# Kernel tuning notes

Measured on AMD Instinct MI355X. Metric: run time of the kernel, lower is better.

Reference implementation:

```python
import math
import jax, jax.numpy as jnp
import numpy as np

IN_CH = 64
NUM_ANCHOR = 4
MAP_H, MAP_W = 96, 96
BATCH = 8
BN_EPS = 1e-5


def _conv2d(x, w, b, padding, dilation):
    # x: [B,C,H,W], w: [O,I,kh,kw] (OIHW)
    y = jax.lax.conv_general_dilated(
        x, w, window_strides=(1, 1),
        padding=((padding, padding), (padding, padding)),
        rhs_dilation=(dilation, dilation),
        dimension_numbers=('NCHW', 'OIHW', 'NCHW'))
    return y + b[None, :, None, None]


def _bn(x, gamma, beta, mean, var):
    scale = gamma / jnp.sqrt(var + BN_EPS)
    return x * scale[None, :, None, None] + (beta - mean * scale)[None, :, None, None]


def setup_inputs() -> dict:
    key = jax.random.key(0)
    ks = jax.random.split(key, 12)
    # cyclic channel-shift permutation matrices, one per anchor pass
    eye = np.eye(IN_CH, dtype=np.float32)
    shift = IN_CH // (2 * NUM_ANCHOR)
    perms = np.stack([eye[np.roll(np.arange(IN_CH), i * shift)] for i in range(2 * NUM_ANCHOR)])
    w_std = 1.0 / math.sqrt(IN_CH * 9)
    return {
        'x': jax.random.normal(ks[0], (BATCH, IN_CH, MAP_H, MAP_W), dtype=jnp.float32),
        'perms': jnp.asarray(perms),
        'dcn_w': jax.random.normal(ks[1], (IN_CH, IN_CH, 3, 3), dtype=jnp.float32) * w_std,
        'dcn_b': jax.random.normal(ks[2], (IN_CH,), dtype=jnp.float32) * 0.01,
        'conv2_w': jax.random.normal(ks[3], (IN_CH, IN_CH, 3, 3), dtype=jnp.float32) * w_std,
        'conv2_b': jax.random.normal(ks[4], (IN_CH,), dtype=jnp.float32) * 0.01,
        'conv3_w': jax.random.normal(ks[5], (IN_CH, IN_CH, 3, 3), dtype=jnp.float32) * w_std,
        'conv3_b': jax.random.normal(ks[6], (IN_CH,), dtype=jnp.float32) * 0.01,
        'bn_gamma': jax.random.uniform(ks[7], (3, IN_CH), dtype=jnp.float32, minval=0.5, maxval=1.5),
        'bn_beta': jax.random.normal(ks[8], (3, IN_CH), dtype=jnp.float32) * 0.1,
        'bn_mean': jax.random.normal(ks[9], (3, IN_CH), dtype=jnp.float32) * 0.1,
        'bn_var': jax.random.uniform(ks[10], (3, IN_CH), dtype=jnp.float32, minval=0.5, maxval=1.5),
    }


def reference(x, perms, dcn_w, dcn_b, conv2_w, conv2_b, conv3_w, conv3_b,
              bn_gamma, bn_beta, bn_mean, bn_var):
    h = x.shape[2]
    pad = math.ceil(h / (2 ** 1.5 + 2))  # 20 for h=96

    def conv_stack(o):
        # DCN at init (zero offsets) == plain 3x3 conv, pad=1
        o = jax.nn.relu(_bn(_conv2d(o, dcn_w, dcn_b, 1, 1), bn_gamma[0], bn_beta[0], bn_mean[0], bn_var[0]))
        o = jax.nn.relu(_bn(_conv2d(o, conv2_w, conv2_b, 2, 2), bn_gamma[1], bn_beta[1], bn_mean[1], bn_var[1]))
        o = jax.nn.relu(_bn(_conv2d(o, conv3_w, conv3_b, 2, 2), bn_gamma[2], bn_beta[2], bn_mean[2], bn_var[2]))
        return o

    outs = []
    for i in range(2 * NUM_ANCHOR):  # fixed small structural loop
        o = jnp.einsum('mn,bnhw->bmhw', perms[i], x)  # channel permutation
        if i % 2 != 0:
            o = jnp.pad(o, ((0, 0), (0, 0), (pad, pad), (pad, pad)))
        o = jnp.rot90(o, k=i % 4, axes=(-2, -1))   # ccw rotate
        o = conv_stack(o)
        o = jnp.rot90(o, k=(-i) % 4, axes=(-2, -1))  # cw rotate back
        if i % 2 != 0:
            H, W = o.shape[-2], o.shape[-1]
            sh, sw = (H - MAP_H) // 2, (W - MAP_W) // 2
            o = o[..., sh:sh + MAP_H, sw:sw + MAP_W]  # center crop
        outs.append(o)
    out_tensor = jnp.concatenate(outs, axis=1)  # [B, 8*C, H, W]
    out = jnp.max(out_tensor, axis=1, keepdims=True)
    # branch_name == 'midpoint', orientational_anchor=False -> clamped sigmoid
    return jnp.clip(jax.nn.sigmoid(out), 1e-4, 1.0 - 1e-4)
```

## Files before the change

### kernel.cpp

```cpp
#include <hip/hip_runtime.h>
#include <math.h>

#define B 8
#define C 64
#define HW 96
#define NWV 36864

typedef __attribute__((ext_vector_type(8)))  short short8;
typedef __attribute__((ext_vector_type(16))) float floatx16;

__device__ __forceinline__ unsigned short f2bf(float f) {
    unsigned int u = __float_as_uint(f);
    unsigned int r = (u + 0x7fffu + ((u >> 16) & 1u)) >> 16;
    return (unsigned short)r;
}

__device__ __forceinline__ void rotmap(int k, int ta, int tb, int& sa, int& sb) {
    switch (k) {
        case 0: sa = ta;     sb = tb;     break;
        case 1: sa = 2 - tb; sb = ta;     break;
        case 2: sa = 2 - ta; sb = 2 - tb; break;
        default: sa = tb;    sb = 2 - ta; break;
    }
}

__global__ void prep_w(const float* __restrict__ dcn_w, const float* __restrict__ c2w,
                       const float* __restrict__ c3w,
                       const float* __restrict__ gamma, const float* __restrict__ var_,
                       unsigned short* __restrict__ Wall) {
    int idx = blockIdx.x * 256 + threadIdx.x;
    if (idx >= 16 * NWV) return;
    int v = idx / NWV, rem = idx % NWV;
    int tap  = rem >> 12;
    int w12  = rem & 4095;
    int ks   = w12 >> 10;
    int cf   = (w12 >> 9) & 1;
    int lane = (w12 >> 3) & 63;
    int j    = w12 & 7;
    int co = cf * 32 + (lane & 31);
    int ci = ks * 16 + (lane >> 5) * 8 + j;
    int ta = tap / 3, tb = tap % 3;
    const float* src; int k, srcci, l;
    if (v < 8)       { k = v & 3;  srcci = (ci + 8 * v) & 63; src = dcn_w; l = 0; }
    else if (v < 12) { k = v - 8;  srcci = ci; src = c2w; l = 1; }
    else             { k = v - 12; srcci = ci; src = c3w; l = 2; }
    int sa, sb; rotmap(k, ta, tb, sa, sb);
    float s = gamma[l * 64 + co] * rsqrtf(var_[l * 64 + co] + 1e-5f);
    Wall[idx] = f2bf(src[((co * 64 + srcci) * 3 + sa) * 3 + sb] * s);
}

__global__ void prep_bias(const float* __restrict__ dcn_b, const float* __restrict__ c2b,
                          const float* __restrict__ c3b,
                          const float* __restrict__ gamma, const float* __restrict__ beta,
                          const float* __restrict__ mean, const float* __restrict__ var_,
                          float* __restrict__ biasg) {
    int t = threadIdx.x;
    if (t < 192) {
        int l = t >> 6, c = t & 63;
        const float* cb = (l == 0) ? dcn_b : ((l == 1) ? c2b : c3b);
        float s = gamma[l * 64 + c] * rsqrtf(var_[l * 64 + c] + 1e-5f);
        biasg[t] = cb[c] * s + beta[l * 64 + c] - mean[l * 64 + c] * s;
    }
}

__global__ __launch_bounds__(256) void prep_x(const float* __restrict__ in,
                                              unsigned short* __restrict__ out) {
    __shared__ float row[64 * 97];
    int by = blockIdx.x;
    int b = by / 96, y = by % 96;
    int t = threadIdx.x;
    for (int e = t; e < 6144; e += 256) {
        int c = e / 96, x = e - c * 96;
        row[c * 97 + x] = in[(((size_t)(b * 64 + c) * 96 + y) * 96) + x];
    }
    __syncthreads();
    for (int e = t; e < 6144; e += 256) {
        int x = e >> 6, c = e & 63;
        out[(((size_t)(b * 96 + y) * 96 + x) << 6) + c] = f2bf(row[c * 97 + x]);
    }
}

__global__ __launch_bounds__(256) void border_clear(unsigned short* __restrict__ buf1) {
    int idx = blockIdx.y;
    int br = (idx >> 3) * 2, b = idx & 7;
    int z = br * 8 + b;
    int i = blockIdx.x * 32 + (threadIdx.x >> 3);
    int g = threadIdx.x & 7;
    int r, c;
    if (i < 416)      { r = i / 104;              c = i % 104; }
    else if (i < 832) { int j = i - 416; r = 100 + j / 104; c = j % 104; }
    else              { int j = i - 832; r = 4 + (j >> 3); int c8 = j & 7;
                        c = (c8 < 4) ? c8 : 92 + c8; }
    uint4 zero = make_uint4(0u, 0u, 0u, 0u);
    *(uint4*)(buf1 + (size_t)z * (104 * 104 * 64) + ((size_t)(r * 104 + c) << 6) + (g << 3)) = zero;
}

__global__ __launch_bounds__(256, 2) void conv1_k(
    const unsigned short* __restrict__ xhwc, unsigned short* __restrict__ buf1,
    const unsigned short* __restrict__ Wall, const float* __restrict__ biasg) {

    __shared__ __align__(16) unsigned short xt[10 * 34 * 64];
    __shared__ __align__(16) unsigned short xpose[256 * 64];

    int zb = blockIdx.z;
    int bq = zb >> 3, b = zb & 7;
    int fy0 = blockIdx.y * 8, fx0 = blockIdx.x * 32;
    int t = threadIdx.x, lane = t & 63, wv = t >> 6;
    int n = lane & 31, kq = lane >> 5;

    const unsigned short* xb = xhwc + ((size_t)b * 96 * 96 << 6);

    for (int e = t; e < 2720; e += 256) {
        int p = e >> 3, g = e & 7;
        int yy = p / 34, xx = p - yy * 34;
        int gy = fy0 - 5 + yy, gx = fx0 - 5 + xx;
        uint4 v = make_uint4(0u, 0u, 0u, 0u);
        if ((unsigned)gy < 96u && (unsigned)gx < 96u)
            v = *(const uint4*)(xb + ((size_t)(gy * 96 + gx) << 6) + (g << 3));
        *(uint4*)(xt + (p << 6) + ((g ^ (xx & 7)) << 3)) = v;
    }

    float4 bv[2][4];
#pragma unroll
    for (int cf = 0; cf < 2; cf++)
#pragma unroll
        for (int rb = 0; rb < 4; rb++)
            bv[cf][rb] = *(const float4*)(biasg + 32 * cf + 8 * rb + 4 * kq);

    __syncthreads();

    for (int j = 0; j < 4; ++j) {
        int br = bq * 4 + j, odd = br & 1;
        int z = br * 8 + b;
        const short8* Ag = (const short8*)(Wall + (size_t)br * NWV);

        floatx16 acc[2][2];
#pragma unroll
        for (int cf = 0; cf < 2; cf++)
#pragma unroll
            for (int pf = 0; pf < 2; pf++)
#pragma unroll
                for (int i = 0; i < 16; i++) acc[cf][pf][i] = 0.f;

#pragma unroll
        for (int ks = 0; ks < 4; ks++) {
#pragma unroll
            for (int tb = 0; tb < 3; tb++) {
                short8 a[3][2];
#pragma unroll
                for (int ta = 0; ta < 3; ta++)
#pragma unroll
                    for (int cf = 0; cf < 2; cf++)
                        a[ta][cf] = Ag[(((ta * 3 + tb) * 4 + ks) * 2 + cf) * 64 + lane];
                int xx = n + tb;
                int g = ((ks * 2 + kq) ^ (xx & 7)) << 3;
                short8 bf[4];
#pragma unroll
                for (int rr = 0; rr < 4; rr++) {
                    int p = (2 * wv + rr) * 34 + xx;
                    bf[rr] = *(const short8*)(xt + (p << 6) + g);
                }
#pragma unroll
                for (int ta = 0; ta < 3; ta++)
#pragma unroll
                    for (int pf = 0; pf < 2; pf++) {
                        int rr = pf + ta;
                        acc[0][pf] = __builtin_amdgcn_mfma_f32_32x32x16_bf16(a[ta][0], bf[rr], acc[0][pf], 0, 0, 0);
                        acc[1][pf] = __builtin_amdgcn_mfma_f32_32x32x16_bf16(a[ta][1], bf[rr], acc[1][pf], 0, 0, 0);
                    }
            }
        }

        __syncthreads();
#pragma unroll
        for (int pf = 0; pf < 2; pf++) {
            int pq = (2 * wv + pf) * 32 + n;
            int key = (pq & 7) << 1;
#pragma unroll
            for (int cf = 0; cf < 2; cf++)
#pragma unroll
                for (int rb = 0; rb < 4; rb++) {
                    int u = kq + 2 * rb + 8 * cf;
                    float v0 = fmaxf(acc[cf][pf][rb * 4 + 0] + bv[cf][rb].x, 0.f);
                    float v1 = fmaxf(acc[cf][pf][rb * 4 + 1] + bv[cf][rb].y, 0.f);
                    float v2 = fmaxf(acc[cf][pf][rb * 4 + 2] + bv[cf][rb].z, 0.f);
                    float v3 = fmaxf(acc[cf][pf][rb * 4 + 3] + bv[cf][rb].w, 0.f);
                    uint2 pk = make_uint2((unsigned)f2bf(v0) | ((unsigned)f2bf(v1) << 16),
                                          (unsigned)f2bf(v2) | ((unsigned)f2bf(v3) << 16));
                    *(uint2*)((char*)xpose + pq * 128 + ((u ^ key) << 3)) = pk;
                }
        }
        __syncthreads();

        unsigned short* fb = buf1 + (size_t)z * (104 * 104 * 64);
        int lo = odd ? 0 : 4, hi = odd ? 104 : 100;
        for (int e = t; e < 2048; e += 256) {
            int px = e >> 3, g = e & 7;
            int key = (px & 7) << 1;
            uint4 v = *(const uint4*)((const char*)xpose + px * 128 + (((2 * g) ^ key) << 3));
            int lr = px >> 5, nn = px & 31;
            int f = fy0 + lr, fc = fx0 + nn;
            if (f >= lo && f < hi && fc >= lo && fc < hi)
                *(uint4*)(fb + ((size_t)(f * 104 + fc) << 6) + (g << 3)) = v;
        }
    }
}

__global__ __launch_bounds__(1024, 4) void conv23_k(
    const unsigned short* __restrict__ buf1, float* __restrict__ maxb,
    const unsigned short* __restrict__ Wall, const float* __restrict__ biasg) {

    __shared__ __align__(16) unsigned short c2out[768 * 64];
    __shared__ __align__(16) unsigned short xs[960 * 32];

    int z = blockIdx.z, br = z >> 3, odd = br & 1;
    int oy0 = blockIdx.y * 16, ox0 = blockIdx.x * 32;
    int t = threadIdx.x, lane = t & 63, wv = t >> 6;
    int n = lane & 31, kq = lane >> 5;

    const unsigned short* fb = buf1 + (size_t)z * (104 * 104 * 64);
    const short8* A2 = (const short8*)(Wall + (size_t)(8  + (br & 3)) * NWV);
    const short8* A3 = (const short8*)(Wall + (size_t)(12 + (br & 3)) * NWV);

    for (int e = t; e < 3840; e += 1024) {
        int p = e >> 2, g = e & 3;
        int yy = p / 40, xx = p - yy * 40;
        uint4 v = *(const uint4*)(fb + ((size_t)((oy0 + yy) * 104 + ox0 + xx) << 6) + (g << 3));
        *(uint4*)(xs + (p << 5) + ((g ^ (xx & 3)) << 3)) = v;
    }
    __syncthreads();

    uint4 pfv[4];
#pragma unroll
    for (int k = 0; k < 4; k++) {
        int e = t + k * 1024;
        if (e < 3840) {
            int p = e >> 2, g = e & 3;
            int yy = p / 40, xx = p - yy * 40;
            pfv[k] = *(const uint4*)(fb + ((size_t)((oy0 + yy) * 104 + ox0 + xx) << 6) + 32 + (g << 3));
        }
    }

    int ch_[2], q_[2], row2_[2], col2_[2];
#pragma unroll
    for (int jj = 0; jj < 2; jj++) {
        int ch = 2 * wv + jj;
        ch_[jj] = ch;
        int q = ch * 32 + n;
        q_[jj] = q;
        int qc = (q < 720) ? q : 719;
        int r2 = qc / 36;
        row2_[jj] = r2;
        col2_[jj] = qc - 36 * r2;
    }

    floatx16 acc2[2][2];
#pragma unroll
    for (int jj = 0; jj < 2; jj++)
#pragma unroll
        for (int cf = 0; cf < 2; cf++)
#pragma unroll
            for (int i = 0; i < 16; i++) acc2[jj][cf][i] = 0.f;

#pragma unroll
    for (int s = 0; s < 2; s++) {
        if (s == 1) {
            __syncthreads();
#pragma unroll
            for (int k = 0; k < 4; k++) {
                int e = t + k * 1024;
                if (e < 3840) {
                    int p = e >> 2, g = e & 3;
                    int xx2 = p - (p / 40) * 40;
                    *(uint4*)(xs + (p << 5) + ((g ^ (xx2 & 3)) << 3)) = pfv[k];
                }
            }
            __syncthreads();
        }
        if (ch_[0] < 23) {
#pragma unroll
            for (int kl = 0; kl < 2; kl++) {
                int ks = s * 2 + kl;
#pragma unroll
                for (int tb = 0; tb < 3; tb++) {
                    short8 a[3][2];
#pragma unroll
                    for (int ta = 0; ta < 3; ta++)
#pragma unroll
                        for (int cf = 0; cf < 2; cf++)
                            a[ta][cf] = A2[(((ta * 3 + tb) * 4 + ks) * 2 + cf) * 64 + lane];
#pragma unroll
                    for (int jj = 0; jj < 2; jj++) {
                        if (ch_[jj] < 23) {
                            int colx = col2_[jj] + 2 * tb;
                            int gsw = ((kl * 2 + kq) ^ (colx & 3)) << 3;
#pragma unroll
                            for (int ta = 0; ta < 3; ta++) {
                                int p = (row2_[jj] + 2 * ta) * 40 + colx;
                                short8 bfr = *(const short8*)(xs + (p << 5) + gsw);
                                acc2[jj][0] = __builtin_amdgcn_mfma_f32_32x32x16_bf16(a[ta][0], bfr, acc2[jj][0], 0, 0, 0);
                                acc2[jj][1] = __builtin_amdgcn_mfma_f32_32x32x16_bf16(a[ta][1], bfr, acc2[jj][1], 0, 0, 0);
                            }
                        }
                    }
                }
            }
        }
    }

    int rlo2 = (!odd && oy0 == 0)  ? 2  : 0;
    int rhi2 = (!odd && oy0 == 80) ? 18 : 20;
    int clo2 = (!odd && ox0 == 0)  ? 2  : 0;
    int chi2 = (!odd && ox0 == 64) ? 34 : 36;
    float4 bv2[2][4];
#pragma unroll
    for (int cf = 0; cf < 2; cf++)
#pragma unroll
        for (int rb = 0; rb < 4; rb++)
            bv2[cf][rb] = *(const float4*)(biasg + 64 + 32 * cf + 8 * rb + 4 * kq);

#pragma unroll
    for (int jj = 0; jj < 2; jj++) {
        if (ch_[jj] < 23 && q_[jj] < 720) {
            bool valid = (row2_[jj] >= rlo2) && (row2_[jj] < rhi2) &&
                         (col2_[jj] >= clo2) && (col2_[jj] < chi2);
            int key = col2_[jj] & 14;
#pragma unroll
            for (int cf = 0; cf < 2; cf++)
#pragma unroll
                for (int rb = 0; rb < 4; rb++) {
                    int u = kq + 2 * rb + 8 * cf;
                    float v0 = 0.f, v1 = 0.f, v2 = 0.f, v3 = 0.f;
                    if (valid) {
                        v0 = fmaxf(acc2[jj][cf][rb * 4 + 0] + bv2[cf][rb].x, 0.f);
                        v1 = fmaxf(acc2[jj][cf][rb * 4 + 1] + bv2[cf][rb].y, 0.f);
                        v2 = fmaxf(acc2[jj][cf][rb * 4 + 2] + bv2[cf][rb].z, 0.f);
                        v3 = fmaxf(acc2[jj][cf][rb * 4 + 3] + bv2[cf][rb].w, 0.f);
                    }
                    uint2 pk = make_uint2((unsigned)f2bf(v0) | ((unsigned)f2bf(v1) << 16),
                                          (unsigned)f2bf(v2) | ((unsigned)f2bf(v3) << 16));
                    *(uint2*)((char*)c2out + q_[jj] * 128 + ((u ^ key) << 3)) = pk;
                }
        }
    }
    __syncthreads();

    int r0 = wv;
    floatx16 acc3[2];
#pragma unroll
    for (int cf = 0; cf < 2; cf++)
#pragma unroll
        for (int i = 0; i < 16; i++) acc3[cf][i] = 0.f;

#pragma unroll
    for (int ks = 0; ks < 4; ks++) {
#pragma unroll
        for (int tb = 0; tb < 3; tb++) {
            short8 a[3][2];
#pragma unroll
            for (int ta = 0; ta < 3; ta++)
#pragma unroll
                for (int cf = 0; cf < 2; cf++)
                    a[ta][cf] = A3[(((ta * 3 + tb) * 4 + ks) * 2 + cf) * 64 + lane];
            int col = n + 2 * tb;
            int key = col & 14;
            int ublk = 2 * (ks * 2 + kq);
            short8 bf[3];
#pragma unroll
            for (int ta = 0; ta < 3; ta++) {
                int q = (r0 + 2 * ta) * 36 + col;
                bf[ta] = *(const short8*)((const char*)c2out + q * 128 + ((ublk ^ key) << 3));
            }
#pragma unroll
            for (int ta = 0; ta < 3; ta++) {
                acc3[0] = __builtin_amdgcn_mfma_f32_32x32x16_bf16(a[ta][0], bf[ta], acc3[0], 0, 0, 0);
                acc3[1] = __builtin_amdgcn_mfma_f32_32x32x16_bf16(a[ta][1], bf[ta], acc3[1], 0, 0, 0);
            }
        }
    }

    float4 bv3[2][4];
#pragma unroll
    for (int cf = 0; cf < 2; cf++)
#pragma unroll
        for (int rb = 0; rb < 4; rb++)
            bv3[cf][rb] = *(const float4*)(biasg + 128 + 32 * cf + 8 * rb + 4 * kq);

    float m = 0.f;
#pragma unroll
    for (int cf = 0; cf < 2; cf++)
#pragma unroll
        for (int rb = 0; rb < 4; rb++) {
            m = fmaxf(m, acc3[cf][rb * 4 + 0] + bv3[cf][rb].x);
            m = fmaxf(m, acc3[cf][rb * 4 + 1] + bv3[cf][rb].y);
            m = fmaxf(m, acc3[cf][rb * 4 + 2] + bv3[cf][rb].z);
            m = fmaxf(m, acc3[cf][rb * 4 + 3] + bv3[cf][rb].w);
        }
    m = fmaxf(m, 0.f);
    m = fmaxf(m, __shfl_xor(m, 32, 64));
    if (lane < 32)
        maxb[((size_t)z * 96 + oy0 + r0) * 96 + ox0 + n] = m;
}

__global__ void final_k(const float* __restrict__ maxb, float* __restrict__ out) {
    int i = blockIdx.x * 256 + threadIdx.x;
    if (i < B * HW * HW) {
        int b = i / 9216, yx = i - b * 9216;
        float m = 0.f;
#pragma unroll
        for (int br = 0; br < 8; br++)
            m = fmaxf(m, maxb[((size_t)(br * 8 + b)) * 9216 + yx]);
        float v = 1.f / (1.f + expf(-m));
        out[i] = fminf(fmaxf(v, 1e-4f), 1.f - 1e-4f);
    }
}


extern "C" void kernel_launch(void* const* d_in, const int* in_sizes, int n_in,
                              void* d_out, int out_size, void* d_ws, size_t ws_size,
                              hipStream_t stream) {
    const float* x     = (const float*)d_in[0];
    const float* dcn_w = (const float*)d_in[2];
    const float* dcn_b = (const float*)d_in[3];
    const float* c2w   = (const float*)d_in[4];
    const float* c2b   = (const float*)d_in[5];
    const float* c3w   = (const float*)d_in[6];
    const float* c3b   = (const float*)d_in[7];
    const float* gamma = (const float*)d_in[8];
    const float* beta  = (const float*)d_in[9];
    const float* mean  = (const float*)d_in[10];
    const float* var_  = (const float*)d_in[11];

    char* ws = (char*)d_ws;
    unsigned short* Wall = (unsigned short*)ws;
    size_t off = (size_t)16 * NWV * 2;
    float* biasg = (float*)(ws + off);            off += 1024;
    float* maxb  = (float*)(ws + off);            off += (size_t)64 * 9216 * 4;
    unsigned short* xhwc = (unsigned short*)(ws + off); off += (size_t)B * 9216 * 64 * 2;
    unsigned short* buf1 = (unsigned short*)(ws + off);

    prep_w<<<(16 * NWV + 255) / 256, 256, 0, stream>>>(dcn_w, c2w, c3w, gamma, var_, Wall);
    prep_bias<<<1, 256, 0, stream>>>(dcn_b, c2b, c3b, gamma, beta, mean, var_, biasg);
    prep_x<<<B * 96, 256, 0, stream>>>(x, xhwc);
    border_clear<<<dim3(50, 32), 256, 0, stream>>>(buf1);

    dim3 g1(4, 13, 16);
    conv1_k<<<g1, 256, 0, stream>>>(xhwc, buf1, Wall, biasg);

    dim3 g23(3, 6, 64);
    conv23_k<<<g23, 1024, 0, stream>>>(buf1, maxb, Wall, biasg);

    final_k<<<(B * HW * HW + 255) / 256, 256, 0, stream>>>(maxb, (float*)d_out);
}
```

Measured before the change: 333.2 us.

## Split conv1 per branch and halve conv23 tile height with shared LDS buffer

conv1 now launches one block per branch instead of looping over four branches per block, and reuses the input tile's LDS for the transpose staging. conv23 drops to 8 output rows per block with 512 threads and aliases the input and conv2-output LDS regions, assigning the extra conv2 row chunks to spare waves. This shrinks per-block LDS to raise occupancy and adds blocks for better CU fill, at the cost of reloading input halos more often and doing relatively more halo conv2 work per output.

```diff
diff --git a/kernel.cpp b/kernel.cpp
--- a/kernel.cpp
+++ b/kernel.cpp
@@ -100,15 +100,14 @@
     const unsigned short* __restrict__ Wall, const float* __restrict__ biasg) {
 
     __shared__ __align__(16) unsigned short xt[10 * 34 * 64];
-    __shared__ __align__(16) unsigned short xpose[256 * 64];
-
-    int zb = blockIdx.z;
-    int bq = zb >> 3, b = zb & 7;
+
+    int z = blockIdx.z, br = z >> 3, b = z & 7, odd = br & 1;
     int fy0 = blockIdx.y * 8, fx0 = blockIdx.x * 32;
     int t = threadIdx.x, lane = t & 63, wv = t >> 6;
     int n = lane & 31, kq = lane >> 5;
 
     const unsigned short* xb = xhwc + ((size_t)b * 96 * 96 << 6);
+    const short8* Ag = (const short8*)(Wall + (size_t)br * NWV);
 
     for (int e = t; e < 2720; e += 256) {
         int p = e >> 3, g = e & 7;
@@ -119,6 +118,44 @@
             v = *(const uint4*)(xb + ((size_t)(gy * 96 + gx) << 6) + (g << 3));
         *(uint4*)(xt + (p << 6) + ((g ^ (xx & 7)) << 3)) = v;
     }
+    __syncthreads();
+
+    floatx16 acc[2][2];
+#pragma unroll
+    for (int cf = 0; cf < 2; cf++)
+#pragma unroll
+        for (int pf = 0; pf < 2; pf++)
+#pragma unroll
+            for (int i = 0; i < 16; i++) acc[cf][pf][i] = 0.f;
+
+#pragma unroll
+    for (int ks = 0; ks < 4; ks++) {
+#pragma unroll
+        for (int tb = 0; tb < 3; tb++) {
+            short8 a[3][2];
+#pragma unroll
+            for (int ta = 0; ta < 3; ta++)
+#pragma unroll
+                for (int cf = 0; cf < 2; cf++)
+                    a[ta][cf] = Ag[(((ta * 3 + tb) * 4 + ks) * 2 + cf) * 64 + lane];
+            int xx = n + tb;
+            int g = ((ks * 2 + kq) ^ (xx & 7)) << 3;
+            short8 bf[4];
+#pragma unroll
+            for (int rr = 0; rr < 4; rr++) {
+                int p = (2 * wv + rr) * 34 + xx;
+                bf[rr] = *(const short8*)(xt + (p << 6) + g);
+            }
+#pragma unroll
+            for (int ta = 0; ta < 3; ta++)
+#pragma unroll
+                for (int pf = 0; pf < 2; pf++) {
+                    int rr = pf + ta;
+                    acc[0][pf] = __builtin_amdgcn_mfma_f32_32x32x16_bf16(a[ta][0], bf[rr], acc[0][pf], 0, 0, 0);
+                    acc[1][pf] = __builtin_amdgcn_mfma_f32_32x32x16_bf16(a[ta][1], bf[rr], acc[1][pf], 0, 0, 0);
+                }
+        }
+    }
 
     float4 bv[2][4];
 #pragma unroll
@@ -128,93 +165,49 @@
             bv[cf][rb] = *(const float4*)(biasg + 32 * cf + 8 * rb + 4 * kq);
 
     __syncthreads();
-
-    for (int j = 0; j < 4; ++j) {
-        int br = bq * 4 + j, odd = br & 1;
-        int z = br * 8 + b;
-        const short8* Ag = (const short8*)(Wall + (size_t)br * NWV);
-
-        floatx16 acc[2][2];
+#pragma unroll
+    for (int pf = 0; pf < 2; pf++) {
+        int pq = (2 * wv + pf) * 32 + n;
+        int key = (pq & 7) << 1;
 #pragma unroll
         for (int cf = 0; cf < 2; cf++)
 #pragma unroll
-            for (int pf = 0; pf < 2; pf++)
-#pragma unroll
-                for (int i = 0; i < 16; i++) acc[cf][pf][i] = 0.f;
-
-#pragma unroll
-        for (int ks = 0; ks < 4; ks++) {
-#pragma unroll
-            for (int tb = 0; tb < 3; tb++) {
-                short8 a[3][2];
-#pragma unroll
-                for (int ta = 0; ta < 3; ta++)
-#pragma unroll
-                    for (int cf = 0; cf < 2; cf++)
-                        a[ta][cf] = Ag[(((ta * 3 + tb) * 4 + ks) * 2 + cf) * 64 + lane];
-                int xx = n + tb;
-                int g = ((ks * 2 + kq) ^ (xx & 7)) << 3;
-                short8 bf[4];
-#pragma unroll
-                for (int rr = 0; rr < 4; rr++) {
-                    int p = (2 * wv + rr) * 34 + xx;
-                    bf[rr] = *(const short8*)(xt + (p << 6) + g);
-                }
-#pragma unroll
-                for (int ta = 0; ta < 3; ta++)
-#pragma unroll
-                    for (int pf = 0; pf < 2; pf++) {
-                        int rr = pf + ta;
-                        acc[0][pf] = __builtin_amdgcn_mfma_f32_32x32x16_bf16(a[ta][0], bf[rr], acc[0][pf], 0, 0, 0);
-                        acc[1][pf] = __builtin_amdgcn_mfma_f32_32x32x16_bf16(a[ta][1], bf[rr], acc[1][pf], 0, 0, 0);
-                    }
-            }
-        }
-
-        __syncthreads();
-#pragma unroll
-        for (int pf = 0; pf < 2; pf++) {
-            int pq = (2 * wv + pf) * 32 + n;
-            int key = (pq & 7) << 1;
-#pragma unroll
-            for (int cf = 0; cf < 2; cf++)
-#pragma unroll
-                for (int rb = 0; rb < 4; rb++) {
-                    int u = kq + 2 * rb + 8 * cf;
-                    float v0 = fmaxf(acc[cf][pf][rb * 4 + 0] + bv[cf][rb].x, 0.f);
-                    float v1 = fmaxf(acc[cf][pf][rb * 4 + 1] + bv[cf][rb].y, 0.f);
-                    float v2 = fmaxf(acc[cf][pf][rb * 4 + 2] + bv[cf][rb].z, 0.f);
-                    float v3 = fmaxf(acc[cf][pf][rb * 4 + 3] + bv[cf][rb].w, 0.f);
-                    uint2 pk = make_uint2((unsigned)f2bf(v0) | ((unsigned)f2bf(v1) << 16),
-                                          (unsigned)f2bf(v2) | ((unsigned)f2bf(v3) << 16));
-                    *(uint2*)((char*)xpose + pq * 128 + ((u ^ key) << 3)) = pk;
-                }
-        }
-        __syncthreads();
-
-        unsigned short* fb = buf1 + (size_t)z * (104 * 104 * 64);
-        int lo = odd ? 0 : 4, hi = odd ? 104 : 100;
-        for (int e = t; e < 2048; e += 256) {
-            int px = e >> 3, g = e & 7;
-            int key = (px & 7) << 1;
-            uint4 v = *(const uint4*)((const char*)xpose + px * 128 + (((2 * g) ^ key) << 3));
-            int lr = px >> 5, nn = px & 31;
-            int f = fy0 + lr, fc = fx0 + nn;
-            if (f >= lo && f < hi && fc >= lo && fc < hi)
-                *(uint4*)(fb + ((size_t)(f * 104 + fc) << 6) + (g << 3)) = v;
-        }
-    }
-}
-
-__global__ __launch_bounds__(1024, 4) void conv23_k(
+            for (int rb = 0; rb < 4; rb++) {
+                int u = kq + 2 * rb + 8 * cf;
+                float v0 = fmaxf(acc[cf][pf][rb * 4 + 0] + bv[cf][rb].x, 0.f);
+                float v1 = fmaxf(acc[cf][pf][rb * 4 + 1] + bv[cf][rb].y, 0.f);
+                float v2 = fmaxf(acc[cf][pf][rb * 4 + 2] + bv[cf][rb].z, 0.f);
+                float v3 = fmaxf(acc[cf][pf][rb * 4 + 3] + bv[cf][rb].w, 0.f);
+                uint2 pk = make_uint2((unsigned)f2bf(v0) | ((unsigned)f2bf(v1) << 16),
+                                      (unsigned)f2bf(v2) | ((unsigned)f2bf(v3) << 16));
+                *(uint2*)((char*)xt + pq * 128 + ((u ^ key) << 3)) = pk;
+            }
+    }
+    __syncthreads();
+
+    unsigned short* fb = buf1 + (size_t)z * (104 * 104 * 64);
+    int lo = odd ? 0 : 4, hi = odd ? 104 : 100;
+    for (int e = t; e < 2048; e += 256) {
+        int px = e >> 3, g = e & 7;
+        int key = (px & 7) << 1;
+        uint4 v = *(const uint4*)((const char*)xt + px * 128 + (((2 * g) ^ key) << 3));
+        int lr = px >> 5, nn = px & 31;
+        int f = fy0 + lr, fc = fx0 + nn;
+        if (f >= lo && f < hi && fc >= lo && fc < hi)
+            *(uint4*)(fb + ((size_t)(f * 104 + fc) << 6) + (g << 3)) = v;
+    }
+}
+
+__global__ __launch_bounds__(512, 4) void conv23_k(
     const unsigned short* __restrict__ buf1, float* __restrict__ maxb,
     const unsigned short* __restrict__ Wall, const float* __restrict__ biasg) {
 
-    __shared__ __align__(16) unsigned short c2out[768 * 64];
-    __shared__ __align__(16) unsigned short xs[960 * 32];
+    __shared__ __align__(16) unsigned char ubuf[432 * 128];
+    unsigned short* xs = (unsigned short*)ubuf;
+    char* c2out = (char*)ubuf;
 
     int z = blockIdx.z, br = z >> 3, odd = br & 1;
-    int oy0 = blockIdx.y * 16, ox0 = blockIdx.x * 32;
+    int oy0 = blockIdx.y * 8, ox0 = blockIdx.x * 32;
     int t = threadIdx.x, lane = t & 63, wv = t >> 6;
     int n = lane & 31, kq = lane >> 5;
 
@@ -222,7 +215,7 @@
     const short8* A2 = (const short8*)(Wall + (size_t)(8  + (br & 3)) * NWV);
     const short8* A3 = (const short8*)(Wall + (size_t)(12 + (br & 3)) * NWV);
 
-    for (int e = t; e < 3840; e += 1024) {
+    for (int e = t; e < 2560; e += 512) {
         int p = e >> 2, g = e & 3;
         int yy = p / 40, xx = p - yy * 40;
         uint4 v = *(const uint4*)(fb + ((size_t)((oy0 + yy) * 104 + ox0 + xx) << 6) + (g << 3));
@@ -230,25 +223,24 @@
     }
     __syncthreads();
 
-    uint4 pfv[4];
-#pragma unroll
-    for (int k = 0; k < 4; k++) {
-        int e = t + k * 1024;
-        if (e < 3840) {
-            int p = e >> 2, g = e & 3;
-            int yy = p / 40, xx = p - yy * 40;
-            pfv[k] = *(const uint4*)(fb + ((size_t)((oy0 + yy) * 104 + ox0 + xx) << 6) + 32 + (g << 3));
-        }
-    }
-
-    int ch_[2], q_[2], row2_[2], col2_[2];
+    uint4 pfv[5];
+#pragma unroll
+    for (int k = 0; k < 5; k++) {
+        int e = t + k * 512;
+        int p = e >> 2, g = e & 3;
+        int yy = p / 40, xx = p - yy * 40;
+        pfv[k] = *(const uint4*)(fb + ((size_t)((oy0 + yy) * 104 + ox0 + xx) << 6) + 32 + (g << 3));
+    }
+
+    int ch_[2];
+    ch_[0] = (wv < 6) ? 2 * wv : (6 + wv);
+    ch_[1] = (wv < 6) ? 2 * wv + 1 : 99;
+    int q_[2], row2_[2], col2_[2];
 #pragma unroll
     for (int jj = 0; jj < 2; jj++) {
-        int ch = 2 * wv + jj;
-        ch_[jj] = ch;
-        int q = ch * 32 + n;
+        int q = ch_[jj] * 32 + n;
         q_[jj] = q;
-        int qc = (q < 720) ? q : 719;
+        int qc = (q < 432) ? q : 431;
         int r2 = qc / 36;
         row2_[jj] = r2;
         col2_[jj] = qc - 36 * r2;
@@ -267,40 +259,36 @@
         if (s == 1) {
             __syncthreads();
 #pragma unroll
-            for (int k = 0; k < 4; k++) {
-                int e = t + k * 1024;
-                if (e < 3840) {
-                    int p = e >> 2, g = e & 3;
-                    int xx2 = p - (p / 40) * 40;
-                    *(uint4*)(xs + (p << 5) + ((g ^ (xx2 & 3)) << 3)) = pfv[k];
-                }
+            for (int k = 0; k < 5; k++) {
+                int e = t + k * 512;
+                int p = e >> 2, g = e & 3;
+                int xx2 = p - (p / 40) * 40;
+                *(uint4*)(xs + (p << 5) + ((g ^ (xx2 & 3)) << 3)) = pfv[k];
             }
             __syncthreads();
         }
-        if (ch_[0] < 23) {
-#pragma unroll
-            for (int kl = 0; kl < 2; kl++) {
-                int ks = s * 2 + kl;
-#pragma unroll
-                for (int tb = 0; tb < 3; tb++) {
-                    short8 a[3][2];
-#pragma unroll
-                    for (int ta = 0; ta < 3; ta++)
-#pragma unroll
-                        for (int cf = 0; cf < 2; cf++)
-                            a[ta][cf] = A2[(((ta * 3 + tb) * 4 + ks) * 2 + cf) * 64 + lane];
-#pragma unroll
-                    for (int jj = 0; jj < 2; jj++) {
-                        if (ch_[jj] < 23) {
-                            int colx = col2_[jj] + 2 * tb;
-                            int gsw = ((kl * 2 + kq) ^ (colx & 3)) << 3;
-#pragma unroll
-                            for (int ta = 0; ta < 3; ta++) {
-                                int p = (row2_[jj] + 2 * ta) * 40 + colx;
-                                short8 bfr = *(const short8*)(xs + (p << 5) + gsw);
-                                acc2[jj][0] = __builtin_amdgcn_mfma_f32_32x32x16_bf16(a[ta][0], bfr, acc2[jj][0], 0, 0, 0);
-                                acc2[jj][1] = __builtin_amdgcn_mfma_f32_32x32x16_bf16(a[ta][1], bfr, acc2[jj][1], 0, 0, 0);
-                            }
+#pragma unroll
+        for (int kl = 0; kl < 2; kl++) {
+            int ks = s * 2 + kl;
+#pragma unroll
+            for (int tb = 0; tb < 3; tb++) {
+                short8 a[3][2];
+#pragma unroll
+                for (int ta = 0; ta < 3; ta++)
+#pragma unroll
+                    for (int cf = 0; cf < 2; cf++)
+                        a[ta][cf] = A2[(((ta * 3 + tb) * 4 + ks) * 2 + cf) * 64 + lane];
+#pragma unroll
+                for (int jj = 0; jj < 2; jj++) {
+                    if (ch_[jj] < 14) {
+                        int colx = col2_[jj] + 2 * tb;
+                        int gsw = ((kl * 2 + kq) ^ (colx & 3)) << 3;
+#pragma unroll
+                        for (int ta = 0; ta < 3; ta++) {
+                            int p = (row2_[jj] + 2 * ta) * 40 + colx;
+                            short8 bfr = *(const short8*)(xs + (p << 5) + gsw);
+                            acc2[jj][0] = __builtin_amdgcn_mfma_f32_32x32x16_bf16(a[ta][0], bfr, acc2[jj][0], 0, 0, 0);
+                            acc2[jj][1] = __builtin_amdgcn_mfma_f32_32x32x16_bf16(a[ta][1], bfr, acc2[jj][1], 0, 0, 0);
                         }
                     }
                 }
@@ -308,8 +296,10 @@
         }
     }
 
+    __syncthreads();
+
     int rlo2 = (!odd && oy0 == 0)  ? 2  : 0;
-    int rhi2 = (!odd && oy0 == 80) ? 18 : 20;
+    int rhi2 = (!odd && oy0 == 88) ? 10 : 12;
     int clo2 = (!odd && ox0 == 0)  ? 2  : 0;
     int chi2 = (!odd && ox0 == 64) ? 34 : 36;
     float4 bv2[2][4];
@@ -321,7 +311,7 @@
 
 #pragma unroll
     for (int jj = 0; jj < 2; jj++) {
-        if (ch_[jj] < 23 && q_[jj] < 720) {
+        if (ch_[jj] < 14 && q_[jj] < 432) {
             bool valid = (row2_[jj] >= rlo2) && (row2_[jj] < rhi2) &&
                          (col2_[jj] >= clo2) && (col2_[jj] < chi2);
             int key = col2_[jj] & 14;
@@ -339,13 +329,12 @@
                     }
                     uint2 pk = make_uint2((unsigned)f2bf(v0) | ((unsigned)f2bf(v1) << 16),
                                           (unsigned)f2bf(v2) | ((unsigned)f2bf(v3) << 16));
-                    *(uint2*)((char*)c2out + q_[jj] * 128 + ((u ^ key) << 3)) = pk;
+                    *(uint2*)(c2out + q_[jj] * 128 + ((u ^ key) << 3)) = pk;
                 }
         }
     }
     __syncthreads();
 
-    int r0 = wv;
     floatx16 acc3[2];
 #pragma unroll
     for (int cf = 0; cf < 2; cf++)
@@ -368,8 +357,8 @@
             short8 bf[3];
 #pragma unroll
             for (int ta = 0; ta < 3; ta++) {
-                int q = (r0 + 2 * ta) * 36 + col;
-                bf[ta] = *(const short8*)((const char*)c2out + q * 128 + ((ublk ^ key) << 3));
+                int q = (wv + 2 * ta) * 36 + col;
+                bf[ta] = *(const short8*)(c2out + q * 128 + ((ublk ^ key) << 3));
             }
 #pragma unroll
             for (int ta = 0; ta < 3; ta++) {
@@ -399,7 +388,7 @@
     m = fmaxf(m, 0.f);
     m = fmaxf(m, __shfl_xor(m, 32, 64));
     if (lane < 32)
-        maxb[((size_t)z * 96 + oy0 + r0) * 96 + ox0 + n] = m;
+        maxb[((size_t)z * 96 + oy0 + wv) * 96 + ox0 + n] = m;
 }
 
 __global__ void final_k(const float* __restrict__ maxb, float* __restrict__ out) {
@@ -444,11 +433,11 @@
     prep_x<<<B * 96, 256, 0, stream>>>(x, xhwc);
     border_clear<<<dim3(50, 32), 256, 0, stream>>>(buf1);
 
-    dim3 g1(4, 13, 16);
+    dim3 g1(4, 13, 64);
     conv1_k<<<g1, 256, 0, stream>>>(xhwc, buf1, Wall, biasg);
 
-    dim3 g23(3, 6, 64);
-    conv23_k<<<g23, 1024, 0, stream>>>(buf1, maxb, Wall, biasg);
+    dim3 g23(3, 12, 64);
+    conv23_k<<<g23, 512, 0, stream>>>(buf1, maxb, Wall, biasg);
 
     final_k<<<(B * HW * HW + 255) / 256, 256, 0, stream>>>(maxb, (float*)d_out);
 }
```

New measurement: 331.8 us. Within noise of the previous version (-0.4%).
